# Kernel optimization log

Measured on AMD Instinct MI355X. Metric: run time of the kernel, lower is better.

Reference implementation:

```python
import jax, jax.numpy as jnp
import numpy as np

N, L, LEADS = 512, 640, 3
COND_DIM, NUM_K, DIM_K = 1, 100, 5
FLAT = 256 * 79  # 20224, from conv stack trace


def _leaky(x):
    return jnp.where(x >= 0, x, 0.2 * x)


def _sn(w, u):
    # PyTorch spectral_norm: one power iteration (u, v detached), sigma = u^T W v
    wm = w.reshape(w.shape[0], -1)
    v = wm.T @ u
    v = v / (jnp.linalg.norm(v) + 1e-12)
    u2 = wm @ v
    u2 = u2 / (jnp.linalg.norm(u2) + 1e-12)
    u2 = jax.lax.stop_gradient(u2)
    v = jax.lax.stop_gradient(v)
    sigma = u2 @ (wm @ v)
    return w / sigma


def _conv1d(x, w, b, stride, pad):
    y = jax.lax.conv_general_dilated(
        x, w, window_strides=(stride,), padding=[(pad, pad)],
        dimension_numbers=('NCH', 'OIH', 'NCH'))
    return y + b[None, :, None]


def setup_inputs() -> dict:
    key = jax.random.key(0)
    ks = jax.random.split(key, 16)
    g = lambda k, shp, s: (jax.random.normal(k, shp, dtype=jnp.float32) * s)
    inp = {
        'ecg': jax.random.normal(ks[0], (N, L, LEADS), dtype=jnp.float32),
        'condition': jax.random.randint(ks[1], (N, 1), 0, 4),
        'w1': g(ks[2], (64, LEADS, 5), 0.2), 'b1': jnp.zeros((64,), jnp.float32),
        'u1': jax.random.normal(ks[3], (64,), dtype=jnp.float32),
        'w2': g(ks[4], (128, 64, 7), 0.05), 'b2': jnp.zeros((128,), jnp.float32),
        'u2': jax.random.normal(ks[5], (128,), dtype=jnp.float32),
        'w3': g(ks[6], (256, 128, 9), 0.03), 'b3': jnp.zeros((256,), jnp.float32),
        'u3': jax.random.normal(ks[7], (256,), dtype=jnp.float32),
        'emb': g(ks[8], (4, COND_DIM), 1.0),
        'cond_w': g(ks[9], (50, COND_DIM), 0.5), 'cond_b': jnp.zeros((50,), jnp.float32),
        'mb_w': g(ks[10], (FLAT, NUM_K * DIM_K), 0.01),
        'fc_w': g(ks[11], (1, FLAT + NUM_K + 50), 0.01), 'fc_b': jnp.zeros((1,), jnp.float32),
    }
    return inp


def reference(ecg, condition, w1, b1, u1, w2, b2, u2, w3, b3, u3,
              emb, cond_w, cond_b, mb_w, fc_w, fc_b):
    # condition embedding -> Linear(cond_dim, 50)
    cemb = emb[condition[:, 0]]                       # [N, cond_dim]
    cond = cemb @ cond_w.T + cond_b                   # [N, 50]

    x = ecg.transpose(0, 2, 1)                        # [N, 3, 640]
    x = _leaky(_conv1d(x, _sn(w1, u1), b1, 2, 4))     # [N, 64, 322]
    x = _leaky(_conv1d(x, _sn(w2, u2), b2, 2, 3))     # [N, 128, 161]
    x = _leaky(_conv1d(x, _sn(w3, u3), b3, 2, 2))     # [N, 256, 79]
    flat = x.reshape(x.shape[0], -1)                  # [N, 20224]

    # minibatch discrimination
    act = (flat @ mb_w).reshape(-1, NUM_K, DIM_K)     # [N, K, D]
    l1 = jnp.abs(act[:, None] - act[None, :]).sum(-1)  # [N, N, K]
    feats = jnp.exp(-l1).sum(axis=1)                  # [N, K]

    out = jnp.concatenate([flat, feats, cond], axis=1)
    return out @ fc_w.T + fc_b                        # [N, 1]
```

## Files before the change

### kernel.cpp

```cpp
#include <hip/hip_runtime.h>
#include <math.h>

#define NB 512
#define LIN 640
#define NLEADS 3
#define L1O 322
#define L2O 161
#define L3O 79
#define C1N 64
#define C2N 128
#define C3N 256
#define FLATSZ 20224
#define NUMK 100
#define DIMK 5
#define SPLITK 16

typedef __attribute__((ext_vector_type(8))) short short8;
typedef __attribute__((ext_vector_type(4))) float f32x4;

__device__ __forceinline__ unsigned short f2bf(float x){
  unsigned u = __builtin_bit_cast(unsigned, x);
  unsigned r = u + 0x7FFFu + ((u >> 16) & 1u);
  return (unsigned short)(r >> 16);
}
__device__ __forceinline__ float bf2f(unsigned short x){
  unsigned u = ((unsigned)x) << 16;
  return __builtin_bit_cast(float, u);
}

__device__ __forceinline__ float block_reduce_sum(float val, float* red){
#pragma unroll
  for(int off=32; off>0; off>>=1) val += __shfl_down(val, off, 64);
  int lane = threadIdx.x & 63;
  int wv = threadIdx.x >> 6;
  if(lane==0) red[wv] = val;
  __syncthreads();
  int nw = blockDim.x >> 6;
  float r = red[0];
  for(int i=1;i<nw;i++) r += red[i];
  __syncthreads();
  return r;
}

__global__ __launch_bounds__(256)
void sn_pass1(const float* __restrict__ w1, const float* __restrict__ u1,
              const float* __restrict__ w2, const float* __restrict__ u2,
              const float* __restrict__ w3, const float* __restrict__ u3,
              float* __restrict__ v_all, float* __restrict__ ss){
  __shared__ float red[4];
  int b = blockIdx.x, tid = threadIdx.x;
  const float* w; const float* u; int O, C, off, c, widx;
  if(b==0){ w=w1; u=u1; O=64;  C=15;   off=0;   c=tid;            widx=0; }
  else if(b<3){ w=w2; u=u2; O=128; C=448; off=16;  c=(b-1)*256+tid; widx=1; }
  else { w=w3; u=u3; O=256; C=1152; off=464; c=(b-3)*256+tid;      widx=2; }
  float vv = 0.f;
  if(c < C){
    for(int o=0;o<O;o+=4){
      vv += w[(o+0)*C+c]*u[o+0] + w[(o+1)*C+c]*u[o+1]
          + w[(o+2)*C+c]*u[o+2] + w[(o+3)*C+c]*u[o+3];
    }
    v_all[off + c] = vv;
  }
  float ps = (c < C) ? vv*vv : 0.f;
  float tot = block_reduce_sum(ps, red);
  if(tid==0) atomicAdd(&ss[widx], tot);
}

__global__ __launch_bounds__(256)
void sn_pass2(const float* __restrict__ w1, const float* __restrict__ w2,
              const float* __restrict__ w3, const float* __restrict__ v_all,
              float* __restrict__ Sun){
  int b = blockIdx.x, tid = threadIdx.x;
  int lane = tid & 63, wv = tid >> 6;
  const float* w; int C, off, o, widx;
  if(b < 16){ w=w1; C=15;   off=0;   o=b*4+wv;      widx=0; }
  else if(b < 48){ w=w2; C=448; off=16;  o=(b-16)*4+wv; widx=1; }
  else { w=w3; C=1152; off=464; o=(b-48)*4+wv;          widx=2; }
  float t = 0.f;
  for(int c=lane; c<C; c+=64) t += w[o*C+c]*v_all[off+c];
#pragma unroll
  for(int s=32; s>0; s>>=1) t += __shfl_down(t, s, 64);
  if(lane==0) atomicAdd(&Sun[widx], t*t);
}

__global__ void sn_final(const float* __restrict__ ss, const float* __restrict__ Sun,
                         float* __restrict__ scale){
  int tid = threadIdx.x;
  if(tid < 3){
    float inv = 1.f/(sqrtf(ss[tid])+1e-12f);
    float S = Sun[tid]*inv*inv;
    scale[tid] = (sqrtf(S)+1e-12f)/S;
  }
}

__global__ void wprep_kernel(const float* __restrict__ w1, const float* __restrict__ w2,
                             const float* __restrict__ w3, const float* __restrict__ scale,
                             unsigned short* __restrict__ w1p, unsigned short* __restrict__ w2p,
                             unsigned short* __restrict__ w3p){
  int idx = blockIdx.x*256 + threadIdx.x;
  float s1 = scale[0], s2 = scale[1], s3 = scale[2];
  if(idx < C1N*32){
    int o = idx >> 5, kk = idx & 31;
    w1p[idx] = (kk < 15) ? f2bf(w1[o*15+kk]*s1) : 0;
  }
  if(idx < C2N*448){
    int o = idx / 448, k2 = idx - o*448;
    int r = k2 >> 6, i = k2 & 63;
    w2p[idx] = f2bf(w2[o*448 + i*7 + r]*s2);
  }
  if(idx < C3N*1152){
    int o = idx / 1152, k2 = idx - o*1152;
    int r = k2 >> 7, i = k2 & 127;
    w3p[idx] = f2bf(w3[o*1152 + i*9 + r]*s3);
  }
}

__global__ __launch_bounds__(256, 4)
void conv12_mfma(const float* __restrict__ ecg, const unsigned short* __restrict__ w1p,
                 const float* __restrict__ b1, const unsigned short* __restrict__ w2p,
                 const float* __restrict__ b2, unsigned short* __restrict__ y2t){
  __shared__ unsigned short slabs[13600];
  __shared__ unsigned short B1s[6656];
  int n = blockIdx.x, tile = blockIdx.y, tid = threadIdx.x;
  int lane = tid & 63, w = tid >> 6;
  int c0    = tile ? 189 : 0;
  int tbase = tile ? 96  : 0;
  int suboff= tile ? -94 : 2;

  {
    uint4 z = {0u,0u,0u,0u};
    uint4* zd = (uint4*)slabs;
#pragma unroll
    for(int q=0;q<7;q++){
      int f = q*256 + tid;
      if(f < 1700) zd[f] = z;
    }
  }
  const float* eb = ecg + (size_t)n*LIN*NLEADS;
#pragma unroll
  for(int q=0;q<26;q++){
    int e = q*256 + tid;
    int tp = e >> 5, kk = e & 31;
    unsigned short v = 0;
    if(kk < 15){
      int i = kk/5, r = kk - i*5;
      int p = 2*(c0 + tp) - 4 + r;
      if((unsigned)p < (unsigned)LIN) v = f2bf(eb[p*NLEADS + i]);
    }
    B1s[tp*32 + kk] = v;
  }
  __syncthreads();

  {
    short8 a1 = *(const short8*)(w1p + ((w*16 + (lane&15))<<5) + (lane>>4)*8);
    f32x4 zero = {0.f,0.f,0.f,0.f};
#pragma unroll
    for(int half=0; half<2; half++){
      int nt0 = half*7, ntc = half ? 6 : 7;
      f32x4 c1[7];
      for(int j=0;j<ntc;j++){
        short8 b = *(const short8*)(B1s + (((nt0+j)*16 + (lane&15))<<5) + (lane>>4)*8);
        c1[j] = __builtin_amdgcn_mfma_f32_16x16x32_bf16(a1, b, zero, 0, 0, 0);
      }
#pragma unroll
      for(int reg=0;reg<4;reg++){
        int o = w*16 + (lane>>4)*4 + reg;
        float bias = b1[o];
        for(int j=0;j<ntc;j++){
          int tp = (nt0+j)*16 + (lane&15);
          int t1 = c0 + tp;
          int sub = (t1>>1) + suboff;
          if(t1 < L1O && sub < 100){
            float v = c1[j][reg] + bias;
            v = v>=0.f ? v : 0.2f*v;
            slabs[((t1&1)?6800:0) + sub*68 + o] = f2bf(v);
          }
        }
      }
    }
  }
  __syncthreads();

  f32x4 zero = {0.f,0.f,0.f,0.f};
  f32x4 acc[2][6];
#pragma unroll
  for(int i=0;i<2;i++)
#pragma unroll
    for(int j=0;j<6;j++) acc[i][j] = zero;

  const unsigned short* w2base = w2p + ((size_t)(w*2*16 + (lane&15)))*448 + (lane>>4)*8;
  short8 a_cur[2];
  a_cur[0] = *(const short8*)(w2base);
  a_cur[1] = *(const short8*)(w2base + 16*448);

  for(int ck=0; ck<14; ck++){
    short8 a_nxt[2];
    if(ck < 13){
      a_nxt[0] = *(const short8*)(w2base + (ck+1)*32);
      a_nxt[1] = *(const short8*)(w2base + 16*448 + (ck+1)*32);
    }
    int r = ck >> 1, i0 = (ck & 1)*32;
    int p = (r+1) & 1;
    int m = ((r-3) - p) >> 1;
    int base = (p?6800:0) + (m+2 + (lane&15))*68 + i0 + (lane>>4)*8;
    short8 b[6];
#pragma unroll
    for(int nt=0;nt<6;nt++)
      b[nt] = *(const short8*)(slabs + base + nt*16*68);
#pragma unroll
    for(int mm=0;mm<2;mm++)
#pragma unroll
      for(int nt=0;nt<6;nt++)
        acc[mm][nt] = __builtin_amdgcn_mfma_f32_16x16x32_bf16(a_cur[mm], b[nt], acc[mm][nt], 0, 0, 0);
    if(ck < 13){ a_cur[0] = a_nxt[0]; a_cur[1] = a_nxt[1]; }
  }

  __syncthreads();
  unsigned short* trans = slabs;
#pragma unroll
  for(int mm=0;mm<2;mm++){
#pragma unroll
    for(int reg=0;reg<4;reg++){
      int o = (w*2+mm)*16 + (lane>>4)*4 + reg;
      float bias = b2[o];
#pragma unroll
      for(int nt=0;nt<6;nt++){
        int tl = nt*16 + (lane&15);
        int t = tbase + tl;
        if(t < L2O){
          float v = acc[mm][nt][reg] + bias;
          v = v>=0.f ? v : 0.2f*v;
          trans[tl*136 + o] = f2bf(v);
        }
      }
    }
  }
  __syncthreads();
  {
    int rows = tile ? 65 : 96;
    uint4* dstg = (uint4*)(y2t + (size_t)n*20608 + tbase*128);
#pragma unroll
    for(int q=0;q<6;q++){
      int f = q*256 + tid;
      int row = f >> 4, c8 = f & 15;
      if(row < rows)
        dstg[row*16 + c8] = *(const uint4*)(trans + row*136 + c8*8);
    }
  }
}

__global__ __launch_bounds__(256, 2)
void conv3_mfma(const unsigned short* __restrict__ y2t, const unsigned short* __restrict__ w3p,
                const float* __restrict__ b3, unsigned short* __restrict__ flatbf){
  __shared__ unsigned short lds[22712];
  int n = blockIdx.x, tid = threadIdx.x;
  int lane = tid & 63, w = tid >> 6;

  if(tid < 136){
    lds[tid] = 0;
    lds[82*136 + tid] = 0;
    lds[83*136 + tid] = 0;
    lds[11424 + tid] = 0;
    lds[11424 + 81*136 + tid] = 0;
    lds[11424 + 82*136 + tid] = 0;
  }
  {
    const uint4* src = (const uint4*)(y2t + (size_t)n*20608);
#pragma unroll
    for(int q=0;q<11;q++){
      int f = q*256 + tid;
      if(f < 2576){
        int g = f >> 4, c8 = f & 15;
        int sub = g >> 1, p = g & 1;
        *(uint4*)(lds + (p ? 11424 : 0) + (sub+1)*136 + c8*8) = src[(size_t)g*16 + c8];
      }
    }
  }

  f32x4 zero = {0.f,0.f,0.f,0.f};
  f32x4 acc[4][5];
#pragma unroll
  for(int i=0;i<4;i++)
#pragma unroll
    for(int j=0;j<5;j++) acc[i][j] = zero;

  const unsigned short* wbase = w3p + ((size_t)(w*64) + (lane&15))*1152 + (lane>>4)*8;
  short8 a_cur[4];
#pragma unroll
  for(int mm=0;mm<4;mm++)
    a_cur[mm] = *(const short8*)(wbase + mm*16*1152);
  __syncthreads();

  for(int ck=0; ck<36; ck++){
    short8 a_nxt[4];
    if(ck < 35){
      int kc = (ck+1)*32;
#pragma unroll
      for(int mm=0;mm<4;mm++)
        a_nxt[mm] = *(const short8*)(wbase + mm*16*1152 + kc);
    }
    int r = ck >> 2, i0 = (ck & 3) * 32;
    int cbase = ((r & 1) ? 11424 : 0) + (r >> 1)*136 + i0 + (lane>>4)*8;
    short8 b[5];
#pragma unroll
    for(int nt=0;nt<5;nt++){
      int t = nt*16 + (lane&15);
      b[nt] = *(const short8*)(lds + cbase + t*136);
    }
#pragma unroll
    for(int mm=0;mm<4;mm++)
#pragma unroll
      for(int nt=0;nt<5;nt++)
        acc[mm][nt] = __builtin_amdgcn_mfma_f32_16x16x32_bf16(a_cur[mm], b[nt], acc[mm][nt], 0, 0, 0);
    if(ck < 35){
#pragma unroll
      for(int mm=0;mm<4;mm++) a_cur[mm] = a_nxt[mm];
    }
  }
#pragma unroll
  for(int mm=0;mm<4;mm++){
#pragma unroll
    for(int reg=0;reg<4;reg++){
      int o = w*64 + mm*16 + (lane>>4)*4 + reg;
      float bias = b3[o];
#pragma unroll
      for(int nt=0;nt<5;nt++){
        int t = nt*16 + (lane&15);
        if(t < L3O){
          float v = acc[mm][nt][reg] + bias;
          v = v>=0.f ? v : 0.2f*v;
          flatbf[(size_t)n*FLATSZ + o*L3O + t] = f2bf(v);
        }
      }
    }
  }
}

__global__ __launch_bounds__(256)
void mbw_transpose(const float* __restrict__ mbw, unsigned short* __restrict__ mbwT){
  __shared__ unsigned short tile[32][36];
  int k0 = blockIdx.x*32, n0 = blockIdx.y*32, tid = threadIdx.x;
  int r = tid >> 3, c4 = (tid & 7) * 4;
  int nbase = n0 + c4;
  if(nbase + 3 < 500){
    float4 v = *(const float4*)(mbw + (size_t)(k0+r)*500 + nbase);
    tile[r][c4+0] = f2bf(v.x);
    tile[r][c4+1] = f2bf(v.y);
    tile[r][c4+2] = f2bf(v.z);
    tile[r][c4+3] = f2bf(v.w);
  } else {
#pragma unroll
    for(int j=0;j<4;j++){
      int nn = nbase + j;
      float v = (nn < 500) ? mbw[(size_t)(k0+r)*500 + nn] : 0.f;
      tile[r][c4+j] = f2bf(v);
    }
  }
  __syncthreads();
  int nl = tid >> 3, kq = (tid & 7) * 4;
  unsigned short t0 = tile[kq+0][nl], t1 = tile[kq+1][nl];
  unsigned short t2 = tile[kq+2][nl], t3 = tile[kq+3][nl];
  uint2 p;
  p.x = (unsigned)t0 | ((unsigned)t1 << 16);
  p.y = (unsigned)t2 | ((unsigned)t3 << 16);
  *(uint2*)(mbwT + (size_t)(n0+nl)*FLATSZ + k0 + kq) = p;
}

__global__ __launch_bounds__(256)
void mb_gemm_mfma(const unsigned short* __restrict__ flatbf, const unsigned short* __restrict__ mbwT,
                  float* __restrict__ part){
  __shared__ unsigned short As[64*32];
  __shared__ unsigned short Bs[64*32];
  int tid = threadIdx.x;
  int lane = tid & 63, w = tid >> 6;
  int m0 = blockIdx.x*64, n0 = blockIdx.y*64, bz = blockIdx.z;
  int t_start = bz*39 + (bz<8 ? bz : 8);
  int t_count = 39 + (bz<8 ? 1 : 0);
  int k0 = t_start*32;
  f32x4 zero = {0.f,0.f,0.f,0.f};
  f32x4 acc[4];
#pragma unroll
  for(int i=0;i<4;i++) acc[i] = zero;
  int arow = tid >> 2, acol = (tid & 3) * 8;
  for(int t=0; t<t_count; t++, k0+=32){
    __syncthreads();
    ((uint4*)As)[tid] = *(const uint4*)(flatbf + (size_t)(m0+arow)*FLATSZ + k0 + acol);
    ((uint4*)Bs)[tid] = *(const uint4*)(mbwT  + (size_t)(n0+arow)*FLATSZ + k0 + acol);
    __syncthreads();
    short8 a = *(const short8*)(As + (w*16 + (lane&15))*32 + (lane>>4)*8);
#pragma unroll
    for(int nt=0;nt<4;nt++){
      short8 b = *(const short8*)(Bs + (nt*16 + (lane&15))*32 + (lane>>4)*8);
      acc[nt] = __builtin_amdgcn_mfma_f32_16x16x32_bf16(a, b, acc[nt], 0, 0, 0);
    }
  }
  float* po = part + (size_t)bz*NB*500;
#pragma unroll
  for(int nt=0;nt<4;nt++){
#pragma unroll
    for(int reg=0;reg<4;reg++){
      int m = m0 + w*16 + (lane>>4)*4 + reg;
      int c = n0 + nt*16 + (lane&15);
      if(c < 500) po[(size_t)m*500 + c] = acc[nt][reg];
    }
  }
}

__global__ void mb_reduce_kernel(const float* __restrict__ part, float* __restrict__ actT){
  int idx = blockIdx.x*256 + threadIdx.x;
  float s = 0.f;
#pragma unroll
  for(int z=0;z<SPLITK;z++) s += part[(size_t)z*NB*500 + idx];
  int n = idx/500, c = idx - n*500;
  actT[(size_t)c*NB + n] = s;
}

__global__ __launch_bounds__(256)
void feats_kernel(const float* __restrict__ actT, float* __restrict__ feats){
  __shared__ float ash[4][50];
  __shared__ float pred[4][4];
  int i0 = blockIdx.x*4, k0 = blockIdx.y*10;
  int tid = threadIdx.x, lane = tid & 63, wv = tid >> 6;
  if(tid < 200){
    int ii = tid/50, c = tid - ii*50;
    ash[ii][c] = actT[(size_t)(k0*5+c)*NB + i0 + ii];
  }
  __syncthreads();
  const float LOG2E = 1.4426950408889634f;
  int j1 = tid, j2 = tid + 256;
  for(int kk=0; kk<10; kk++){
    const float* r0 = actT + (size_t)(k0+kk)*5*NB;
    float xa0=r0[j1], xa1=r0[NB+j1], xa2=r0[2*NB+j1], xa3=r0[3*NB+j1], xa4=r0[4*NB+j1];
    float xb0=r0[j2], xb1=r0[NB+j2], xb2=r0[2*NB+j2], xb3=r0[3*NB+j2], xb4=r0[4*NB+j2];
    float f[4];
#pragma unroll
    for(int ii=0; ii<4; ii++){
      float a0=ash[ii][kk*5+0], a1=ash[ii][kk*5+1], a2=ash[ii][kk*5+2],
            a3=ash[ii][kk*5+3], a4=ash[ii][kk*5+4];
      float la = fabsf(xa0-a0)+fabsf(xa1-a1)+fabsf(xa2-a2)+fabsf(xa3-a3)+fabsf(xa4-a4);
      float lb = fabsf(xb0-a0)+fabsf(xb1-a1)+fabsf(xb2-a2)+fabsf(xb3-a3)+fabsf(xb4-a4);
      f[ii] = exp2f(-LOG2E*la) + exp2f(-LOG2E*lb);
    }
#pragma unroll
    for(int ii=0; ii<4; ii++){
      float v = f[ii];
#pragma unroll
      for(int s=32; s>0; s>>=1) v += __shfl_down(v, s, 64);
      if(lane==0) pred[wv][ii] = v;
    }
    __syncthreads();
    if(tid < 4){
      float v = pred[0][tid] + pred[1][tid] + pred[2][tid] + pred[3][tid];
      feats[(size_t)(i0+tid)*NUMK + k0 + kk] = v;
    }
    __syncthreads();
  }
}

__global__ void final_kernel(const unsigned short* __restrict__ flatbf, const float* __restrict__ feats,
                             const int* __restrict__ condition, const float* __restrict__ emb,
                             const float* __restrict__ cond_w, const float* __restrict__ cond_b,
                             const float* __restrict__ fc_w, const float* __restrict__ fc_b,
                             float* __restrict__ out){
  __shared__ float red[4];
  int n = blockIdx.x, tid = threadIdx.x;
  float s = 0.f;
  const unsigned short* fr = flatbf + (size_t)n*FLATSZ;
  for(int q=tid; q<FLATSZ/8; q+=256){
    uint4 u = *(const uint4*)(fr + q*8);
    float4 wa = *(const float4*)(fc_w + q*8);
    float4 wb = *(const float4*)(fc_w + q*8 + 4);
    s += bf2f((unsigned short)(u.x & 0xffff))*wa.x + bf2f((unsigned short)(u.x >> 16))*wa.y
       + bf2f((unsigned short)(u.y & 0xffff))*wa.z + bf2f((unsigned short)(u.y >> 16))*wa.w
       + bf2f((unsigned short)(u.z & 0xffff))*wb.x + bf2f((unsigned short)(u.z >> 16))*wb.y
       + bf2f((unsigned short)(u.w & 0xffff))*wb.z + bf2f((unsigned short)(u.w >> 16))*wb.w;
  }
  for(int k=tid;k<NUMK;k+=256) s += feats[n*NUMK+k]*fc_w[FLATSZ+k];
  float ce = emb[condition[n]];
  for(int j=tid;j<50;j+=256) s += (ce*cond_w[j]+cond_b[j])*fc_w[FLATSZ+NUMK+j];
  s = block_reduce_sum(s, red);
  if(tid==0) out[n] = s + fc_b[0];
}

extern "C" void kernel_launch(void* const* d_in, const int* in_sizes, int n_in,
                              void* d_out, int out_size, void* d_ws, size_t ws_size,
                              hipStream_t stream) {
  const float* ecg   = (const float*)d_in[0];
  const int*   cond  = (const int*)  d_in[1];
  const float* w1    = (const float*)d_in[2];
  const float* b1    = (const float*)d_in[3];
  const float* u1    = (const float*)d_in[4];
  const float* w2    = (const float*)d_in[5];
  const float* b2    = (const float*)d_in[6];
  const float* u2    = (const float*)d_in[7];
  const float* w3    = (const float*)d_in[8];
  const float* b3    = (const float*)d_in[9];
  const float* u3    = (const float*)d_in[10];
  const float* emb   = (const float*)d_in[11];
  const float* condw = (const float*)d_in[12];
  const float* condb = (const float*)d_in[13];
  const float* mbw   = (const float*)d_in[14];
  const float* fcw   = (const float*)d_in[15];
  const float* fcb   = (const float*)d_in[16];

  float* ws = (float*)d_ws;
  float* scale = ws;
  float* ssbuf = ws + 16;
  float* Sunbuf= ws + 24;
  float* v_all = ws + 32;
  unsigned short* w1p  = (unsigned short*)(ws + 1648);
  unsigned short* w2p  = (unsigned short*)(ws + 2672);
  unsigned short* w3p  = (unsigned short*)(ws + 31344);
  unsigned short* y2t  = (unsigned short*)(ws + 178800);
  unsigned short* mbwT = (unsigned short*)(ws + 178800);
  float* part  = ws + 5454448;
  float* actT  = ws + 9550448;
  float* feats = ws + 9806448;
  unsigned short* flatbf = (unsigned short*)(ws + 9857648);

  hipMemsetAsync((char*)d_ws + 64, 0, 64, stream);
  sn_pass1<<<8, 256, 0, stream>>>(w1,u1,w2,u2,w3,u3, v_all, ssbuf);
  sn_pass2<<<112, 256, 0, stream>>>(w1,w2,w3, v_all, Sunbuf);
  sn_final<<<1, 64, 0, stream>>>(ssbuf, Sunbuf, scale);
  wprep_kernel<<<1152, 256, 0, stream>>>(w1, w2, w3, scale, w1p, w2p, w3p);
  conv12_mfma<<<dim3(NB,2), 256, 0, stream>>>(ecg, w1p, b1, w2p, b2, y2t);
  conv3_mfma<<<NB, 256, 0, stream>>>(y2t, w3p, b3, flatbf);
  mbw_transpose<<<dim3(632,16), 256, 0, stream>>>(mbw, mbwT);
  mb_gemm_mfma<<<dim3(8,8,SPLITK), 256, 0, stream>>>(flatbf, mbwT, part);
  mb_reduce_kernel<<<1000, 256, 0, stream>>>(part, actT);
  feats_kernel<<<dim3(128,10), 256, 0, stream>>>(actT, feats);
  final_kernel<<<NB, 256, 0, stream>>>(flatbf, feats, cond, emb, condw, condb, fcw, fcb, (float*)d_out);
}
```

Measured before the change: 298.0 us.

## Split conv3 per-sample work into two output-time halves across blocks

conv3_mfma now launches two blocks per sample. Each block loads only the input rows its half of the output positions needs into a smaller LDS buffer and computes 3 or 2 N-tiles through a templated core. The smaller LDS footprint and higher launch-bounds occupancy are meant to give more concurrent blocks and better latency hiding. The cost is duplicated weight loads from global memory and some overlapping halo input rows per block, plus an uneven 3-versus-2 tile split between the halves.

```diff
diff --git a/kernel.cpp b/kernel.cpp
--- a/kernel.cpp
+++ b/kernel.cpp
@@ -249,40 +249,16 @@
   }
 }
 
-__global__ __launch_bounds__(256, 2)
-void conv3_mfma(const unsigned short* __restrict__ y2t, const unsigned short* __restrict__ w3p,
-                const float* __restrict__ b3, unsigned short* __restrict__ flatbf){
-  __shared__ unsigned short lds[22712];
-  int n = blockIdx.x, tid = threadIdx.x;
-  int lane = tid & 63, w = tid >> 6;
-
-  if(tid < 136){
-    lds[tid] = 0;
-    lds[82*136 + tid] = 0;
-    lds[83*136 + tid] = 0;
-    lds[11424 + tid] = 0;
-    lds[11424 + 81*136 + tid] = 0;
-    lds[11424 + 82*136 + tid] = 0;
-  }
-  {
-    const uint4* src = (const uint4*)(y2t + (size_t)n*20608);
-#pragma unroll
-    for(int q=0;q<11;q++){
-      int f = q*256 + tid;
-      if(f < 2576){
-        int g = f >> 4, c8 = f & 15;
-        int sub = g >> 1, p = g & 1;
-        *(uint4*)(lds + (p ? 11424 : 0) + (sub+1)*136 + c8*8) = src[(size_t)g*16 + c8];
-      }
-    }
-  }
-
+template<int NT>
+__device__ __forceinline__ void conv3_core(const unsigned short* lds, const unsigned short* __restrict__ w3p,
+                                           const float* __restrict__ b3, unsigned short* __restrict__ flatbf,
+                                           int n, int tb, int lane, int w){
   f32x4 zero = {0.f,0.f,0.f,0.f};
-  f32x4 acc[4][5];
+  f32x4 acc[4][NT];
 #pragma unroll
   for(int i=0;i<4;i++)
 #pragma unroll
-    for(int j=0;j<5;j++) acc[i][j] = zero;
+    for(int j=0;j<NT;j++) acc[i][j] = zero;
 
   const unsigned short* wbase = w3p + ((size_t)(w*64) + (lane&15))*1152 + (lane>>4)*8;
   short8 a_cur[4];
@@ -300,17 +276,17 @@
         a_nxt[mm] = *(const short8*)(wbase + mm*16*1152 + kc);
     }
     int r = ck >> 2, i0 = (ck & 3) * 32;
-    int cbase = ((r & 1) ? 11424 : 0) + (r >> 1)*136 + i0 + (lane>>4)*8;
-    short8 b[5];
-#pragma unroll
-    for(int nt=0;nt<5;nt++){
+    int cbase = ((r & 1) ? 7072 : 0) + (r >> 1)*136 + i0 + (lane>>4)*8;
+    short8 b[NT];
+#pragma unroll
+    for(int nt=0;nt<NT;nt++){
       int t = nt*16 + (lane&15);
       b[nt] = *(const short8*)(lds + cbase + t*136);
     }
 #pragma unroll
     for(int mm=0;mm<4;mm++)
 #pragma unroll
-      for(int nt=0;nt<5;nt++)
+      for(int nt=0;nt<NT;nt++)
         acc[mm][nt] = __builtin_amdgcn_mfma_f32_16x16x32_bf16(a_cur[mm], b[nt], acc[mm][nt], 0, 0, 0);
     if(ck < 35){
 #pragma unroll
@@ -324,8 +300,8 @@
       int o = w*64 + mm*16 + (lane>>4)*4 + reg;
       float bias = b3[o];
 #pragma unroll
-      for(int nt=0;nt<5;nt++){
-        int t = nt*16 + (lane&15);
+      for(int nt=0;nt<NT;nt++){
+        int t = tb + nt*16 + (lane&15);
         if(t < L3O){
           float v = acc[mm][nt][reg] + bias;
           v = v>=0.f ? v : 0.2f*v;
@@ -334,6 +310,47 @@
       }
     }
   }
+}
+
+__global__ __launch_bounds__(256, 4)
+void conv3_mfma(const unsigned short* __restrict__ y2t, const unsigned short* __restrict__ w3p,
+                const float* __restrict__ b3, unsigned short* __restrict__ flatbf){
+  __shared__ unsigned short lds[14144];
+  int n = blockIdx.x, h = blockIdx.y, tid = threadIdx.x;
+  int lane = tid & 63, w = tid >> 6;
+
+  if(tid < 136){
+    if(h == 0){
+      lds[tid] = 0;
+      lds[7072 + tid] = 0;
+    } else {
+      lds[34*136 + tid] = 0;
+      lds[35*136 + tid] = 0;
+      lds[7072 + 33*136 + tid] = 0;
+      lds[7072 + 34*136 + tid] = 0;
+      lds[7072 + 35*136 + tid] = 0;
+    }
+  }
+  {
+    int g0    = h ? 94 : 0;
+    int nrows = h ? 67 : 102;
+    int roff  = h ? -47 : 1;
+    const uint4* src = (const uint4*)(y2t + (size_t)n*20608 + (size_t)g0*128);
+#pragma unroll
+    for(int q=0;q<7;q++){
+      int f = q*256 + tid;
+      if(f < nrows*16){
+        int g_rel = f >> 4, c8 = f & 15;
+        int g = g0 + g_rel;
+        int lr = (g >> 1) + roff;
+        int p = g & 1;
+        *(uint4*)(lds + (p ? 7072 : 0) + lr*136 + c8*8) = src[(size_t)g_rel*16 + c8];
+      }
+    }
+  }
+
+  if(h == 0) conv3_core<3>(lds, w3p, b3, flatbf, n, 0,  lane, w);
+  else       conv3_core<2>(lds, w3p, b3, flatbf, n, 48, lane, w);
 }
 
 __global__ __launch_bounds__(256)
@@ -524,7 +541,7 @@
   sn_final<<<1, 64, 0, stream>>>(ssbuf, Sunbuf, scale);
   wprep_kernel<<<1152, 256, 0, stream>>>(w1, w2, w3, scale, w1p, w2p, w3p);
   conv12_mfma<<<dim3(NB,2), 256, 0, stream>>>(ecg, w1p, b1, w2p, b2, y2t);
-  conv3_mfma<<<NB, 256, 0, stream>>>(y2t, w3p, b3, flatbf);
+  conv3_mfma<<<dim3(NB,2), 256, 0, stream>>>(y2t, w3p, b3, flatbf);
   mbw_transpose<<<dim3(632,16), 256, 0, stream>>>(mbw, mbwT);
   mb_gemm_mfma<<<dim3(8,8,SPLITK), 256, 0, stream>>>(flatbf, mbwT, part);
   mb_reduce_kernel<<<1000, 256, 0, stream>>>(part, actT);
```

After: 340.7 us. 14.3% more time.
